# Optimization experiments

Measured on AMD Instinct MI355X. Metric: run time of the kernel, lower is better.

## Reference

```python
import jax, jax.numpy as jnp
import numpy as np

NUM_HEADS = 8
NUM_GROUPS = 8
EPS = 1e-5

def group_norm(x, scale, bias):
    b, c, h, w = x.shape
    xg = x.reshape(b, NUM_GROUPS, c // NUM_GROUPS, h, w)
    mean = xg.mean(axis=(2, 3, 4), keepdims=True)
    var = xg.var(axis=(2, 3, 4), keepdims=True)
    xn = ((xg - mean) / jnp.sqrt(var + EPS)).reshape(b, c, h, w)
    return xn * scale[None, :, None, None] + bias[None, :, None, None]

def setup_inputs() -> dict:
    key = jax.random.key(0)
    ks = jax.random.split(key, 7)
    C = 512
    x = jax.random.normal(ks[0], (16, C, 32, 32), dtype=jnp.float32)
    gn_scale = jnp.ones((C,), jnp.float32)
    gn_bias = jnp.zeros((C,), jnp.float32)
    w_qkv = jax.random.normal(ks[1], (3 * C, C), dtype=jnp.float32) * (1.0 / np.sqrt(C))
    b_qkv = jax.random.normal(ks[2], (3 * C,), dtype=jnp.float32) * 0.01
    w_proj = jax.random.normal(ks[3], (C, C), dtype=jnp.float32) * (1.0 / np.sqrt(C))
    b_proj = jax.random.normal(ks[4], (C,), dtype=jnp.float32) * 0.01
    return {"x": x, "gn_scale": gn_scale, "gn_bias": gn_bias,
            "w_qkv": w_qkv, "b_qkv": b_qkv, "w_proj": w_proj, "b_proj": b_proj}

def reference(x, gn_scale, gn_bias, w_qkv, b_qkv, w_proj, b_proj):
    b, c, h, w = x.shape
    hd = c // NUM_HEADS
    hn = group_norm(x, gn_scale, gn_bias)
    # 1x1 conv == per-pixel linear: [b,3c,h,w]
    qkv = jnp.einsum('oc,bchw->bohw', w_qkv, hn) + b_qkv[None, :, None, None]
    q, k, v = jnp.split(qkv, 3, axis=1)
    # -> [b, heads, seq, head_dim], seq = h*w
    def to_heads(t):
        return t.reshape(b, NUM_HEADS, hd, h * w).transpose(0, 1, 3, 2)
    q, k, v = to_heads(q), to_heads(k), to_heads(v)
    scale = 1.0 / jnp.sqrt(jnp.asarray(hd, x.dtype))
    attn = jnp.einsum('bnqd,bnkd->bnqk', q, k) * scale
    attn = jax.nn.softmax(attn, axis=-1)
    out = jnp.einsum('bnqk,bnkd->bnqd', attn, v)
    out = out.transpose(0, 1, 3, 2).reshape(b, c, h, w)
    out = jnp.einsum('oc,bchw->bohw', w_proj, out) + b_proj[None, :, None, None]
    return x + out
```

## Files before the change

kernel.cpp:

```cpp
#include <hip/hip_runtime.h>

typedef _Float16 half8 __attribute__((ext_vector_type(8)));
typedef _Float16 half4 __attribute__((ext_vector_type(4)));
typedef float f32x4 __attribute__((ext_vector_type(4)));

__device__ inline unsigned short f2h(float f) {
  union { _Float16 h; unsigned short u; } cv;
  cv.h = (_Float16)f;
  return cv.u;
}

__device__ inline unsigned int pk2(float a, float b) {
  return __builtin_bit_cast(unsigned int, __builtin_amdgcn_cvt_pkrtz(a, b));
}

__device__ inline void gload_lds16(const void* g, void* l) {
  __builtin_amdgcn_global_load_lds(
      (const __attribute__((address_space(1))) void*)g,
      (__attribute__((address_space(3))) void*)l, 16, 0, 0);
}

__global__ __launch_bounds__(256) void prep(const float* __restrict__ wqkv,
                                            const float* __restrict__ wproj,
                                            _Float16* __restrict__ wq,
                                            _Float16* __restrict__ wp,
                                            const float* __restrict__ x,
                                            float* __restrict__ mr) {
  if (blockIdx.x < 768) {
    const int i = blockIdx.x * 256 + threadIdx.x;
    const float4 v = ((const float4*)wqkv)[i];
    ushort4 pk;
    pk.x = f2h(v.x); pk.y = f2h(v.y); pk.z = f2h(v.z); pk.w = f2h(v.w);
    *(ushort4*)(wq + (size_t)i * 4) = pk;
    if (i < 65536) {
      const float4 u = ((const float4*)wproj)[i];
      ushort4 pu;
      pu.x = f2h(u.x); pu.y = f2h(u.y); pu.z = f2h(u.z); pu.w = f2h(u.w);
      *(ushort4*)(wp + (size_t)i * 4) = pu;
    }
    return;
  }
  const int sb = blockIdx.x - 768;
  const float4* xv = (const float4*)(x + (size_t)sb * 32768);
  float s = 0.f, s2 = 0.f;
  for (int i = threadIdx.x; i < 8192; i += 256) {
    float4 v = xv[i];
    s += v.x + v.y + v.z + v.w;
    s2 += v.x * v.x + v.y * v.y + v.z * v.z + v.w * v.w;
  }
  for (int m = 32; m; m >>= 1) {
    s += __shfl_down(s, m);
    s2 += __shfl_down(s2, m);
  }
  __shared__ float ls[4], ls2[4];
  const int wid = threadIdx.x >> 6;
  if ((threadIdx.x & 63) == 0) { ls[wid] = s; ls2[wid] = s2; }
  __syncthreads();
  if (threadIdx.x == 0) {
    mr[sb * 2] = ls[0] + ls[1] + ls[2] + ls[3];
    mr[sb * 2 + 1] = ls2[0] + ls2[1] + ls2[2] + ls2[3];
  }
}

__global__ __launch_bounds__(256) void gn_apply(const float* __restrict__ x,
                                                const float* __restrict__ mr,
                                                const float* __restrict__ sc,
                                                const float* __restrict__ bi,
                                                _Float16* __restrict__ hn) {
  __shared__ __align__(16) _Float16 t[64][72];
  const int b = blockIdx.z, cb = blockIdx.y, pb = blockIdx.x;
  const int c0 = cb * 64, p0 = pb * 64;
  const int bg = b * 8 + cb;
  const float S = mr[bg * 4 + 0] + mr[bg * 4 + 2];
  const float S2 = mr[bg * 4 + 1] + mr[bg * 4 + 3];
  const float mean = S * (1.f / 65536.f);
  const float var = S2 * (1.f / 65536.f) - mean * mean;
  const float rstd = rsqrtf(var + 1e-5f);
  const int tp = threadIdx.x & 63;
  const int tc = threadIdx.x >> 6;
#pragma unroll
  for (int i = 0; i < 16; i++) {
    const int c = tc * 16 + i;
    const float g = sc[c0 + c] * rstd;
    const float v = x[((size_t)b * 512 + c0 + c) * 1024 + p0 + tp];
    t[tp][c] = (_Float16)((v - mean) * g + bi[c0 + c]);
  }
  __syncthreads();
  const int wp = threadIdx.x >> 2;
  const int wc = (threadIdx.x & 3) * 16;
  _Float16* dst = hn + ((size_t)b * 1024 + p0 + wp) * 512 + c0 + wc;
  *(uint4*)dst = *(const uint4*)&t[wp][wc];
  *(uint4*)(dst + 8) = *(const uint4*)&t[wp][wc + 8];
}

template <int EPI>
__global__ __launch_bounds__(512, 4) void gemm_mfma(
    const _Float16* __restrict__ A, const _Float16* __restrict__ Bt,
    const float* __restrict__ bias, const float* __restrict__ xin,
    float* __restrict__ fout, _Float16* __restrict__ qo,
    _Float16* __restrict__ ko, _Float16* __restrict__ vo) {
  __shared__ __align__(16) _Float16 As[128 * 64];
  __shared__ __align__(16) _Float16 Bs[128 * 64];
  const int b = blockIdx.z;
  const int m0 = blockIdx.y * 128, n0 = blockIdx.x * 128;
  const char* Ab = (const char*)A;
  const char* Bb = (const char*)(Bt + (size_t)b * 1024 * 512);
  const int t = threadIdx.x, lane = t & 63, w = t >> 6;
  const int wm = (w & 1) * 64, wn = (w >> 1) * 32;
  const int lr = lane & 15, lk = lane >> 4;
  int srow[2], scb[2];
#pragma unroll
  for (int it = 0; it < 2; it++) {
    srow[it] = it * 64 + (t >> 3);
    scb[it] = ((t & 7) * 16) ^ ((srow[it] & 7) << 4);
  }
  f32x4 acc[4][2] = {};
#pragma unroll 1
  for (int k0 = 0; k0 < 512; k0 += 64) {
#pragma unroll
    for (int it = 0; it < 2; it++) {
      const size_t go = (size_t)(m0 + srow[it]) * 1024 + k0 * 2 + scb[it];
      const size_t gob = (size_t)(n0 + srow[it]) * 1024 + k0 * 2 + scb[it];
      gload_lds16(Ab + go, (char*)As + it * 8192 + w * 1024);
      gload_lds16(Bb + gob, (char*)Bs + it * 8192 + w * 1024);
    }
    __syncthreads();
#pragma unroll
    for (int kk = 0; kk < 2; kk++) {
      half8 af[4], bf[2];
#pragma unroll
      for (int i = 0; i < 4; i++) {
        const int ra = wm + i * 16 + lr;
        af[i] = *(const half8*)((const char*)As +
                                ((ra * 128 + kk * 64 + lk * 16) ^ ((ra & 7) << 4)));
      }
#pragma unroll
      for (int j = 0; j < 2; j++) {
        const int rb = wn + j * 16 + lr;
        bf[j] = *(const half8*)((const char*)Bs +
                                ((rb * 128 + kk * 64 + lk * 16) ^ ((rb & 7) << 4)));
      }
#pragma unroll
      for (int i = 0; i < 4; i++)
#pragma unroll
        for (int j = 0; j < 2; j++)
          acc[i][j] = __builtin_amdgcn_mfma_f32_16x16x32_f16(af[i], bf[j],
                                                             acc[i][j], 0, 0, 0);
    }
    __syncthreads();
  }
#pragma unroll
  for (int i = 0; i < 4; i++) {
    const int o = m0 + wm + i * 16 + lk * 4;
#pragma unroll
    for (int j = 0; j < 2; j++) {
      const int p = n0 + wn + j * 16 + lr;
      float vv[4];
#pragma unroll
      for (int r = 0; r < 4; r++) vv[r] = acc[i][j][r] + bias[o + r];
      if (EPI == 0) {
        const int sec = o >> 9, oc = o & 511;
        const int h = oc >> 6, d0 = oc & 63;
        if (sec == 0) {
          const float qs = 0.125f * 1.44269504f;
          ushort4 pk;
          pk.x = f2h(vv[0] * qs); pk.y = f2h(vv[1] * qs);
          pk.z = f2h(vv[2] * qs); pk.w = f2h(vv[3] * qs);
          *(ushort4*)(qo + ((size_t)(b * 8 + h) * 1024 + p) * 64 + d0) = pk;
        } else if (sec == 1) {
          ushort4 pk;
          pk.x = f2h(vv[0]); pk.y = f2h(vv[1]);
          pk.z = f2h(vv[2]); pk.w = f2h(vv[3]);
          *(ushort4*)(ko + ((size_t)(b * 8 + h) * 1024 + p) * 64 + d0) = pk;
        } else {
#pragma unroll
          for (int r = 0; r < 4; r++)
            vo[((size_t)(b * 8 + h) * 64 + d0 + r) * 1024 + p] = (_Float16)vv[r];
        }
      } else {
        const size_t idx = ((size_t)b * 512 + o) * 1024 + p;
#pragma unroll
        for (int r = 0; r < 4; r++)
          fout[idx + (size_t)r * 1024] = xin[idx + (size_t)r * 1024] + vv[r];
      }
    }
  }
}

__global__ __launch_bounds__(512, 4) void attn(const _Float16* __restrict__ q,
                                               const _Float16* __restrict__ k,
                                               const _Float16* __restrict__ v,
                                               _Float16* __restrict__ o) {
  __shared__ __align__(16) _Float16 KT[2][4096];
  __shared__ __align__(16) _Float16 VT[2][4096];
  __shared__ __align__(16) _Float16 PT[8][2048];
  const int id = blockIdx.x;
  const int flat = (id & 7) * 64 + (id >> 3);
  const int qb = flat & 3, bh = flat >> 2;
  const int b = bh >> 3, h = bh & 7;
  const int t = threadIdx.x, lane = t & 63, w = t >> 6;
  const int lr = lane & 15, lk = lane >> 4;
  const int q0 = qb * 256 + w * 32;
  const _Float16* qp = q + (size_t)bh * 65536;
  const char* kc = (const char*)(k + (size_t)bh * 65536);
  const char* vc = (const char*)(v + (size_t)bh * 65536);
  const int srow = t >> 3, scol = (t & 7) * 16;
  const int sdst = srow * 128 + (scol ^ ((srow & 7) << 4));
  int koff[4][2];
#pragma unroll
  for (int j = 0; j < 4; j++) {
    const int row = j * 16 + lr, sw = (row & 7) << 4;
    koff[j][0] = row * 128 + ((lk * 16) ^ sw);
    koff[j][1] = row * 128 + ((64 + lk * 16) ^ sw);
  }
  int pwoff[2][4];
#pragma unroll
  for (int g = 0; g < 2; g++) {
    const int qhat = g * 16 + lr, sw = (qhat & 7) << 4;
#pragma unroll
    for (int j = 0; j < 4; j++)
      pwoff[g][j] = qhat * 128 + ((j * 32 + lk * 8) ^ sw);
  }
  half8 qf[2][2];
#pragma unroll
  for (int g = 0; g < 2; g++)
#pragma unroll
    for (int kk = 0; kk < 2; kk++)
      qf[g][kk] = *(const half8*)(qp + (q0 + g * 16 + lr) * 64 + kk * 32 + lk * 8);
  const half8 onesv = {(_Float16)1.f, (_Float16)1.f, (_Float16)1.f, (_Float16)1.f,
                       (_Float16)1.f, (_Float16)1.f, (_Float16)1.f, (_Float16)1.f};
  {
    uint4 k0 = *(const uint4*)(kc + srow * 128 + scol);
    uint4 v0 = *(const uint4*)(vc + srow * 2048 + scol);
    *(uint4*)((char*)KT + sdst) = k0;
    *(uint4*)((char*)VT + sdst) = v0;
  }
  __syncthreads();
  f32x4 aco[2][4] = {};
  f32x4 lacc[2] = {};
  char* Pc = (char*)PT + w * 4096;
#pragma unroll 1
  for (int kt = 0; kt < 16; kt++) {
    const int cur = kt & 1;
    const char* Kc = (const char*)KT + cur * 8192;
    const char* Vc = (const char*)VT + cur * 8192;
    uint4 kn, vn;
    if (kt < 15) {
      kn = *(const uint4*)(kc + (kt + 1) * 8192 + srow * 128 + scol);
      vn = *(const uint4*)(vc + srow * 2048 + (kt + 1) * 128 + scol);
    }
    f32x4 s[2][4];
#pragma unroll
    for (int g = 0; g < 2; g++)
#pragma unroll
      for (int j = 0; j < 4; j++) {
        s[g][j][0] = -10.f; s[g][j][1] = -10.f;
        s[g][j][2] = -10.f; s[g][j][3] = -10.f;
      }
    __builtin_amdgcn_s_setprio(1);
#pragma unroll
    for (int j = 0; j < 4; j++) {
      const half8 kf0 = *(const half8*)(Kc + koff[j][0]);
      const half8 kf1 = *(const half8*)(Kc + koff[j][1]);
#pragma unroll
      for (int g = 0; g < 2; g++) {
        s[g][j] = __builtin_amdgcn_mfma_f32_16x16x32_f16(kf0, qf[g][0], s[g][j], 0, 0, 0);
        s[g][j] = __builtin_amdgcn_mfma_f32_16x16x32_f16(kf1, qf[g][1], s[g][j], 0, 0, 0);
      }
    }
    __builtin_amdgcn_s_setprio(0);
#pragma unroll
    for (int g = 0; g < 2; g++) {
#pragma unroll
      for (int j = 0; j < 4; j++) {
        uint2 pw;
        pw.x = pk2(__builtin_amdgcn_exp2f(s[g][j][0]),
                   __builtin_amdgcn_exp2f(s[g][j][1]));
        pw.y = pk2(__builtin_amdgcn_exp2f(s[g][j][2]),
                   __builtin_amdgcn_exp2f(s[g][j][3]));
        *(uint2*)(Pc + pwoff[g][j]) = pw;
      }
    }
    __builtin_amdgcn_s_setprio(1);
#pragma unroll
    for (int kk = 0; kk < 2; kk++) {
      half8 vf[4];
#pragma unroll
      for (int jd = 0; jd < 4; jd++)
        vf[jd] = *(const half8*)(Vc + koff[jd][kk]);
#pragma unroll
      for (int g = 0; g < 2; g++) {
        const half8 pf = *(const half8*)(Pc + koff[g][kk]);
        lacc[g] = __builtin_amdgcn_mfma_f32_16x16x32_f16(pf, onesv, lacc[g], 0, 0, 0);
#pragma unroll
        for (int jd = 0; jd < 4; jd++)
          aco[g][jd] = __builtin_amdgcn_mfma_f32_16x16x32_f16(pf, vf[jd], aco[g][jd], 0, 0, 0);
      }
    }
    __builtin_amdgcn_s_setprio(0);
    if (kt < 15) {
      *(uint4*)((char*)KT + (cur ^ 1) * 8192 + sdst) = kn;
      *(uint4*)((char*)VT + (cur ^ 1) * 8192 + sdst) = vn;
    }
    __syncthreads();
  }
#pragma unroll
  for (int g = 0; g < 2; g++)
#pragma unroll
    for (int r = 0; r < 4; r++) {
      const float rl = 1.f / lacc[g][r];
      const int row = q0 + g * 16 + 4 * lk + r;
#pragma unroll
      for (int jd = 0; jd < 4; jd++)
        o[((size_t)b * 1024 + row) * 512 + h * 64 + jd * 16 + lr] =
            (_Float16)(aco[g][jd][r] * rl);
    }
}

extern "C" void kernel_launch(void* const* d_in, const int* in_sizes, int n_in,
                              void* d_out, int out_size, void* d_ws, size_t ws_size,
                              hipStream_t stream) {
  const float* x = (const float*)d_in[0];
  const float* gsc = (const float*)d_in[1];
  const float* gbi = (const float*)d_in[2];
  const float* wqkv = (const float*)d_in[3];
  const float* bqkv = (const float*)d_in[4];
  const float* wproj = (const float*)d_in[5];
  const float* bproj = (const float*)d_in[6];
  float* out = (float*)d_out;
  char* ws = (char*)d_ws;
  float* mr = (float*)ws;
  _Float16* wq16 = (_Float16*)(ws + 4096);
  _Float16* wp16 = (_Float16*)(ws + 4096 + 1572864);
  _Float16* hn = (_Float16*)(ws + 2101248);
  _Float16* q16 = (_Float16*)(ws + 18878464);
  _Float16* k16 = (_Float16*)(ws + 35655680);
  _Float16* v16 = (_Float16*)(ws + 52432896);

  hipLaunchKernelGGL(prep, dim3(1024), dim3(256), 0, stream, wqkv, wproj, wq16,
                     wp16, x, mr);
  hipLaunchKernelGGL(gn_apply, dim3(16, 8, 16), dim3(256), 0, stream, x, mr, gsc,
                     gbi, hn);
  hipLaunchKernelGGL((gemm_mfma<0>), dim3(8, 12, 16), dim3(512), 0, stream, wq16,
                     hn, bqkv, (const float*)nullptr, (float*)nullptr, q16, k16,
                     v16);
  hipLaunchKernelGGL(attn, dim3(512), dim3(512), 0, stream, q16, k16, v16, hn);
  hipLaunchKernelGGL((gemm_mfma<1>), dim3(8, 4, 16), dim3(512), 0, stream, wp16,
                     hn, bproj, x, out, (_Float16*)nullptr, (_Float16*)nullptr,
                     (_Float16*)nullptr);
}
```

Baseline: 128.0 us.

## Double-buffer LDS tiles in GEMM to overlap global loads with MFMA

The GEMM kernel now uses two LDS buffers for A and B tiles, prefetching the tile two steps ahead while computing on the current one. It replaces full __syncthreads with explicit vmcnt waits and s_barrier so outstanding loads can stay in flight across barriers. This is meant to hide global-to-LDS load latency behind the MFMA work. It doubles LDS usage per block, which may reduce how many blocks fit per CU.

```diff
diff --git a/kernel.cpp b/kernel.cpp
--- a/kernel.cpp
+++ b/kernel.cpp
@@ -99,8 +99,8 @@
     const float* __restrict__ bias, const float* __restrict__ xin,
     float* __restrict__ fout, _Float16* __restrict__ qo,
     _Float16* __restrict__ ko, _Float16* __restrict__ vo) {
-  __shared__ __align__(16) _Float16 As[128 * 64];
-  __shared__ __align__(16) _Float16 Bs[128 * 64];
+  __shared__ __align__(16) _Float16 As[2][128 * 64];
+  __shared__ __align__(16) _Float16 Bs[2][128 * 64];
   const int b = blockIdx.z;
   const int m0 = blockIdx.y * 128, n0 = blockIdx.x * 128;
   const char* Ab = (const char*)A;
@@ -115,29 +115,35 @@
     scb[it] = ((t & 7) * 16) ^ ((srow[it] & 7) << 4);
   }
   f32x4 acc[4][2] = {};
+#pragma unroll
+  for (int kp = 0; kp < 2; kp++) {
+#pragma unroll
+    for (int it = 0; it < 2; it++) {
+      const size_t go = (size_t)(m0 + srow[it]) * 1024 + kp * 128 + scb[it];
+      const size_t gob = (size_t)(n0 + srow[it]) * 1024 + kp * 128 + scb[it];
+      gload_lds16(Ab + go, (char*)As[kp] + it * 8192 + w * 1024);
+      gload_lds16(Bb + gob, (char*)Bs[kp] + it * 8192 + w * 1024);
+    }
+  }
+  asm volatile("s_waitcnt vmcnt(4)" ::: "memory");
+  __builtin_amdgcn_s_barrier();
+  asm volatile("" ::: "memory");
 #pragma unroll 1
-  for (int k0 = 0; k0 < 512; k0 += 64) {
-#pragma unroll
-    for (int it = 0; it < 2; it++) {
-      const size_t go = (size_t)(m0 + srow[it]) * 1024 + k0 * 2 + scb[it];
-      const size_t gob = (size_t)(n0 + srow[it]) * 1024 + k0 * 2 + scb[it];
-      gload_lds16(Ab + go, (char*)As + it * 8192 + w * 1024);
-      gload_lds16(Bb + gob, (char*)Bs + it * 8192 + w * 1024);
-    }
-    __syncthreads();
+  for (int ks = 0; ks < 8; ks++) {
+    const int cur = ks & 1;
 #pragma unroll
     for (int kk = 0; kk < 2; kk++) {
       half8 af[4], bf[2];
 #pragma unroll
       for (int i = 0; i < 4; i++) {
         const int ra = wm + i * 16 + lr;
-        af[i] = *(const half8*)((const char*)As +
+        af[i] = *(const half8*)((const char*)As[cur] +
                                 ((ra * 128 + kk * 64 + lk * 16) ^ ((ra & 7) << 4)));
       }
 #pragma unroll
       for (int j = 0; j < 2; j++) {
         const int rb = wn + j * 16 + lr;
-        bf[j] = *(const half8*)((const char*)Bs +
+        bf[j] = *(const half8*)((const char*)Bs[cur] +
                                 ((rb * 128 + kk * 64 + lk * 16) ^ ((rb & 7) << 4)));
       }
 #pragma unroll
@@ -147,7 +153,26 @@
           acc[i][j] = __builtin_amdgcn_mfma_f32_16x16x32_f16(af[i], bf[j],
                                                              acc[i][j], 0, 0, 0);
     }
-    __syncthreads();
+    if (ks == 7) break;
+    asm volatile("" ::: "memory");
+    __builtin_amdgcn_s_barrier();
+    asm volatile("" ::: "memory");
+    if (ks + 2 < 8) {
+#pragma unroll
+      for (int it = 0; it < 2; it++) {
+        const size_t go =
+            (size_t)(m0 + srow[it]) * 1024 + (ks + 2) * 128 + scb[it];
+        const size_t gob =
+            (size_t)(n0 + srow[it]) * 1024 + (ks + 2) * 128 + scb[it];
+        gload_lds16(Ab + go, (char*)As[cur] + it * 8192 + w * 1024);
+        gload_lds16(Bb + gob, (char*)Bs[cur] + it * 8192 + w * 1024);
+      }
+      asm volatile("s_waitcnt vmcnt(4)" ::: "memory");
+    } else {
+      asm volatile("s_waitcnt vmcnt(0)" ::: "memory");
+    }
+    __builtin_amdgcn_s_barrier();
+    asm volatile("" ::: "memory");
   }
 #pragma unroll
   for (int i = 0; i < 4; i++) {
```

Result: no change. 127.2 us (-0.6%).
